# Kernel optimization log

Hardware: AMD Instinct MI355X
Metric: run time of the kernel (lower is better)

## Reference

```python
import jax, jax.numpy as jnp
import numpy as np

N = 50000
E = 800000
F_IN = 128
HID = 128
H_HID = 4
H_OUT = 6
N_CLS = 40
NEG_SLOPE = 0.2
BN_EPS = 1e-5


def gat_conv(x, src, dst, W, a_src, a_dst, bias, concat):
    # x: [N, F_in]; W: [F_in, H*C]; a_src/a_dst: [H, C]
    H, C = a_src.shape
    h = (x @ W).reshape(N, H, C)                      # [N,H,C]
    alpha_s = jnp.sum(h * a_src[None], axis=-1)       # [N,H]
    alpha_d = jnp.sum(h * a_dst[None], axis=-1)       # [N,H]
    e = jax.nn.leaky_relu(alpha_s[src] + alpha_d[dst], NEG_SLOPE)  # [E',H]
    # segment softmax over incoming edges of each dst node
    emax = jax.ops.segment_max(e, dst, num_segments=N)
    e = jnp.exp(e - emax[dst])
    denom = jax.ops.segment_sum(e, dst, num_segments=N)
    alpha = e / (denom[dst] + 1e-16)                  # [E',H]
    out = jax.ops.segment_sum(alpha[:, :, None] * h[src], dst, num_segments=N)  # [N,H,C]
    out = out.reshape(N, H * C) if concat else out.mean(axis=1)
    return out + bias


def bn_eval(x, gamma, beta, mean, var):
    return (x - mean) * (gamma / jnp.sqrt(var + BN_EPS)) + beta


def setup_inputs() -> dict:
    key = jax.random.key(0)
    ks = jax.random.split(key, 24)
    d_h = HID * H_HID  # 512
    inp = {
        'x': jax.random.normal(ks[0], (N, F_IN), jnp.float32),
        'edge_index': jax.random.randint(ks[1], (2, E), 0, N, jnp.int64),
        # layer 0: GATConv(128 -> 128, heads=4, concat)
        'W0': jax.random.normal(ks[2], (F_IN, d_h), jnp.float32) * 0.1,
        'as0': jax.random.normal(ks[3], (H_HID, HID), jnp.float32) * 0.1,
        'ad0': jax.random.normal(ks[4], (H_HID, HID), jnp.float32) * 0.1,
        'b0': jnp.zeros((d_h,), jnp.float32),
        'g0': jax.random.uniform(ks[5], (d_h,), jnp.float32, 0.5, 1.5),
        'bt0': jax.random.normal(ks[6], (d_h,), jnp.float32) * 0.1,
        'm0': jax.random.normal(ks[7], (d_h,), jnp.float32) * 0.1,
        'v0': jax.random.uniform(ks[8], (d_h,), jnp.float32, 0.5, 1.5),
        # layer 1: GATConv(512 -> 128, heads=4, concat)
        'W1': jax.random.normal(ks[9], (d_h, d_h), jnp.float32) * 0.05,
        'as1': jax.random.normal(ks[10], (H_HID, HID), jnp.float32) * 0.1,
        'ad1': jax.random.normal(ks[11], (H_HID, HID), jnp.float32) * 0.1,
        'b1': jnp.zeros((d_h,), jnp.float32),
        'g1': jax.random.uniform(ks[12], (d_h,), jnp.float32, 0.5, 1.5),
        'bt1': jax.random.normal(ks[13], (d_h,), jnp.float32) * 0.1,
        'm1': jax.random.normal(ks[14], (d_h,), jnp.float32) * 0.1,
        'v1': jax.random.uniform(ks[15], (d_h,), jnp.float32, 0.5, 1.5),
        # layer 2: GATConv(512 -> 40, heads=6, concat=False)
        'W2': jax.random.normal(ks[16], (d_h, H_OUT * N_CLS), jnp.float32) * 0.05,
        'as2': jax.random.normal(ks[17], (H_OUT, N_CLS), jnp.float32) * 0.1,
        'ad2': jax.random.normal(ks[18], (H_OUT, N_CLS), jnp.float32) * 0.1,
        'b2': jnp.zeros((N_CLS,), jnp.float32),
    }
    return inp


def reference(x, edge_index, W0, as0, ad0, b0, g0, bt0, m0, v0,
              W1, as1, ad1, b1, g1, bt1, m1, v1,
              W2, as2, ad2, b2):
    # add self loops (PyG GATConv default add_self_loops=True)
    loop = jnp.arange(N, dtype=edge_index.dtype)
    src = jnp.concatenate([edge_index[0], loop])
    dst = jnp.concatenate([edge_index[1], loop])
    # dropout is a no-op in eval mode
    h = gat_conv(x, src, dst, W0, as0, ad0, b0, concat=True)
    h = jax.nn.elu(bn_eval(h, g0, bt0, m0, v0))
    h = gat_conv(h, src, dst, W1, as1, ad1, b1, concat=True)
    h = jax.nn.elu(bn_eval(h, g1, bt1, m1, v1))
    h = gat_conv(h, src, dst, W2, as2, ad2, b2, concat=False)
    return jax.nn.log_softmax(h, axis=-1)
```

## Files before the change

### kernel.cpp

```cpp
#include <hip/hip_runtime.h>
#include <cstdint>
#include <cstddef>

#define NN 50000
#define EE 800000
#define EPQ (EE + NN)
#define NEG_SLOPE 0.2f
#define BN_EPS 1e-5f
#define SCB 256
#define NBLK ((NN + SCB - 1) / SCB)

typedef _Float16 f16x8 __attribute__((ext_vector_type(8)));
typedef _Float16 f16x4 __attribute__((ext_vector_type(4)));
typedef _Float16 f16x2 __attribute__((ext_vector_type(2)));
typedef float f32x4 __attribute__((ext_vector_type(4)));
typedef float f32x2 __attribute__((ext_vector_type(2)));
typedef unsigned int u32;
typedef unsigned char u8;
typedef unsigned short u16;

static __device__ __forceinline__ float lrelu(float x) { return x > 0.f ? x : x * NEG_SLOPE; }

static __device__ __forceinline__ u8 f32_to_fp8(float v) {
    return (u8)(__builtin_amdgcn_cvt_pk_fp8_f32(v, v, 0, false) & 0xff);
}
static __device__ __forceinline__ void fp8x4_to_f32(u32 v, float* o) {
    f32x2 lo = __builtin_amdgcn_cvt_pk_f32_fp8(v, false);
    f32x2 hi = __builtin_amdgcn_cvt_pk_f32_fp8(v, true);
    o[0] = lo[0]; o[1] = lo[1]; o[2] = hi[0]; o[3] = hi[1];
}

static __device__ __forceinline__ void gld_lds16(const void* g, void* l) {
    __builtin_amdgcn_global_load_lds((const __attribute__((address_space(1))) u32*)g,
                                     (__attribute__((address_space(3))) u32*)l, 16, 0, 0);
}

__global__ void init_count(int* __restrict__ count) {
    int i = blockIdx.x * blockDim.x + threadIdx.x;
    if (i < NN) count[i] = 1;
}

__global__ void hist_kernel(const int* __restrict__ dst, int* __restrict__ count) {
    int e = blockIdx.x * blockDim.x + threadIdx.x;
    if (e < EE) atomicAdd(&count[dst[e]], 1);
}

__global__ __launch_bounds__(SCB) void scan1(const int* __restrict__ count,
                                             int* __restrict__ excl, int* __restrict__ bsum) {
    __shared__ int tmp[SCB];
    int b = blockIdx.x, t = threadIdx.x;
    int i = b * SCB + t;
    int v = (i < NN) ? count[i] : 0;
    tmp[t] = v;
    __syncthreads();
    for (int off = 1; off < SCB; off <<= 1) {
        int u = (t >= off) ? tmp[t - off] : 0;
        __syncthreads();
        tmp[t] += u;
        __syncthreads();
    }
    if (i < NN) excl[i] = tmp[t] - v;
    if (t == SCB - 1) bsum[b] = tmp[t];
}

__global__ __launch_bounds__(256) void scan2(const int* __restrict__ bsum, int* __restrict__ boff) {
    __shared__ int tmp[256];
    int t = threadIdx.x;
    int v = (t < NBLK) ? bsum[t] : 0;
    tmp[t] = v;
    __syncthreads();
    for (int off = 1; off < 256; off <<= 1) {
        int u = (t >= off) ? tmp[t - off] : 0;
        __syncthreads();
        tmp[t] += u;
        __syncthreads();
    }
    boff[t] = tmp[t] - v;
}

__global__ void scan3(const int* __restrict__ excl, const int* __restrict__ boff,
                      int* __restrict__ rowptr, int* __restrict__ cursor) {
    int i = blockIdx.x * blockDim.x + threadIdx.x;
    if (i < NN) {
        int r = excl[i] + boff[i / SCB];
        rowptr[i] = r;
        cursor[i] = r;
    }
    if (i == NN) rowptr[NN] = EPQ;
}

__global__ void scatter_kernel(const int* __restrict__ src, const int* __restrict__ dst,
                               int* __restrict__ cursor, int* __restrict__ csrs) {
    int e = blockIdx.x * blockDim.x + threadIdx.x;
    if (e < EE) {
        int d = dst[e];
        int slot = atomicAdd(&cursor[d], 1);
        csrs[slot] = src[e];
    } else if (e < EPQ) {
        int i = e - EE;
        int slot = atomicAdd(&cursor[i], 1);
        csrs[slot] = i;
    }
}

__global__ void cast_x_kernel(const float* __restrict__ in, _Float16* __restrict__ out,
                              u32* __restrict__ outq, int n4) {
    int i = blockIdx.x * blockDim.x + threadIdx.x;
    if (i >= n4) return;
    f32x4 v = *(const f32x4*)(in + (size_t)i * 4);
    f16x4 o;
    o[0] = (_Float16)v[0]; o[1] = (_Float16)v[1]; o[2] = (_Float16)v[2]; o[3] = (_Float16)v[3];
    *(f16x4*)(out + (size_t)i * 4) = o;
    u32 q = __builtin_amdgcn_cvt_pk_fp8_f32(v[0], v[1], 0, false);
    q = __builtin_amdgcn_cvt_pk_fp8_f32(v[2], v[3], q, true);
    outq[i] = q;
}

__global__ __launch_bounds__(256) void tcast_kernel(const float* __restrict__ W,
                                                    _Float16* __restrict__ Wt, int K, int Nc) {
    __shared__ float tile[32][33];
    int bx = blockIdx.x * 32;
    int by = blockIdx.y * 32;
    int tx = threadIdx.x & 31, ty = threadIdx.x >> 5;
#pragma unroll
    for (int r = 0; r < 32; r += 8) {
        int k = by + ty + r, n = bx + tx;
        tile[ty + r][tx] = (k < K && n < Nc) ? W[(size_t)k * Nc + n] : 0.f;
    }
    __syncthreads();
#pragma unroll
    for (int r = 0; r < 32; r += 8) {
        int n = bx + ty + r, k = by + tx;
        if (n < Nc && k < K) Wt[(size_t)n * K + k] = (_Float16)tile[tx][ty + r];
    }
}

__global__ void prep_bn(const float* g0, const float* bt0, const float* m0, const float* v0,
                        const float* b0, const float* g1, const float* bt1, const float* m1,
                        const float* v1, const float* b1, float* sc01, float* sh01) {
    int t = threadIdx.x;
    const float *g, *bt, *m, *v, *b;
    int c;
    if (t < 512) { g = g0; bt = bt0; m = m0; v = v0; b = b0; c = t; }
    else         { g = g1; bt = bt1; m = m1; v = v1; b = b1; c = t - 512; }
    float s = g[c] * rsqrtf(v[c] + BN_EPS);
    sc01[t] = s;
    sh01[t] = (b[c] - m[c]) * s + bt[c];
}

__global__ __launch_bounds__(512) void prep_va(const _Float16* __restrict__ W0t,
                                               const _Float16* __restrict__ W1t,
                                               const _Float16* __restrict__ W2t,
                                               const float* __restrict__ as0,
                                               const float* __restrict__ ad0,
                                               const float* __restrict__ as1,
                                               const float* __restrict__ ad1,
                                               const float* __restrict__ as2,
                                               const float* __restrict__ ad2,
                                               float* __restrict__ va0, float* __restrict__ va1,
                                               float* __restrict__ va2) {
    int bid = blockIdx.x, t = threadIdx.x;
    if (bid < 8) {
        if (t >= 128) return;
        int j = bid, h = j & 3;
        const float* a = (j < 4 ? as0 : ad0) + h * 128;
        float s = 0.f;
        for (int c = 0; c < 128; c++) s += (float)W0t[(size_t)(h * 128 + c) * 128 + t] * a[c];
        va0[j * 128 + t] = s;
    } else if (bid < 16) {
        int j = bid - 8, h = j & 3;
        const float* a = (j < 4 ? as1 : ad1) + h * 128;
        float s = 0.f;
        for (int c = 0; c < 128; c++) s += (float)W1t[(size_t)(h * 128 + c) * 512 + t] * a[c];
        va1[j * 512 + t] = s;
    } else {
        int j = bid - 16, h = j % 6;
        const float* a = (j < 6 ? as2 : ad2) + h * 40;
        float s = 0.f;
        for (int c = 0; c < 40; c++) s += (float)W2t[(size_t)(h * 40 + c) * 512 + t] * a[c];
        va2[j * 512 + t] = s;
    }
}

template <bool BD, bool EPI, int OT>
__global__ __launch_bounds__(256) void gemm_t(const _Float16* __restrict__ A, int lda,
                                              const _Float16* __restrict__ Bt,
                                              void* __restrict__ Cv, int ldc, int M, int Nc,
                                              int K, const float* __restrict__ sc,
                                              const float* __restrict__ sh) {
    __shared__ __align__(16) _Float16 As[2][128 * 64];
    __shared__ __align__(16) _Float16 Bs[2][128 * 64];
    const int t = threadIdx.x;
    const int bm = blockIdx.x * 128;
    const int bn = blockIdx.y * 128;
    const int wid = t >> 6, lane = t & 63;
    const int wm = (wid >> 1) * 64, wn = (wid & 1) * 64;
    const int aoff = BD ? bn : 0;
    f32x4 acc[4][4] = {};
    const int nsteps = K >> 6;

    auto STAGE = [&](int buf, int k0) {
#pragma unroll
        for (int it = 0; it < 4; ++it) {
            int rbase = it * 32 + wid * 8;
            int row = rbase + (lane >> 3);
            int c8g = (lane & 7) ^ (row & 7);
            gld_lds16(A + (size_t)(bm + row) * lda + aoff + k0 + c8g * 8,
                      (char*)As[buf] + rbase * 128);
            gld_lds16(Bt + (size_t)(bn + row) * K + k0 + c8g * 8, (char*)Bs[buf] + rbase * 128);
        }
    };

    STAGE(0, 0);
    __syncthreads();
    int cur = 0;
    for (int s = 0; s < nsteps; ++s) {
        if (s + 1 < nsteps) STAGE(cur ^ 1, (s + 1) * 64);
#pragma unroll
        for (int ks = 0; ks < 2; ++ks) {
            f16x8 af[4], bf[4];
#pragma unroll
            for (int mi = 0; mi < 4; ++mi) {
                int row = wm + mi * 16 + (lane & 15);
                int c8 = (ks * 4 + (lane >> 4)) ^ (row & 7);
                af[mi] = *(const f16x8*)((const char*)As[cur] + row * 128 + c8 * 16);
            }
#pragma unroll
            for (int ni = 0; ni < 4; ++ni) {
                int row = wn + ni * 16 + (lane & 15);
                int c8 = (ks * 4 + (lane >> 4)) ^ (row & 7);
                bf[ni] = *(const f16x8*)((const char*)Bs[cur] + row * 128 + c8 * 16);
            }
#pragma unroll
            for (int mi = 0; mi < 4; ++mi)
#pragma unroll
                for (int ni = 0; ni < 4; ++ni)
                    acc[mi][ni] = __builtin_amdgcn_mfma_f32_16x16x32_f16(af[mi], bf[ni],
                                                                         acc[mi][ni], 0, 0, 0);
        }
        __syncthreads();
        cur ^= 1;
    }
    float scv[4], shv[4];
    if (EPI) {
#pragma unroll
        for (int ni = 0; ni < 4; ++ni) {
            int gcol = bn + wn + ni * 16 + (lane & 15);
            scv[ni] = sc[gcol];
            shv[ni] = sh[gcol];
        }
    }
#pragma unroll
    for (int mi = 0; mi < 4; ++mi) {
#pragma unroll
        for (int r = 0; r < 4; ++r) {
            int grow = bm + wm + mi * 16 + (lane >> 4) * 4 + r;
            if (grow < M) {
#pragma unroll
                for (int ni = 0; ni < 4; ++ni) {
                    int gcol = bn + wn + ni * 16 + (lane & 15);
                    if (gcol < Nc) {
                        float v = acc[mi][ni][r];
                        if (EPI) {
                            v = v * scv[ni] + shv[ni];
                            v = v > 0.f ? v : expm1f(v);
                        }
                        if constexpr (OT == 0) {
                            ((_Float16*)Cv)[(size_t)grow * ldc + gcol] = (_Float16)v;
                        } else {
                            ((u8*)Cv)[(size_t)grow * ldc + gcol] = f32_to_fp8(v);
                        }
                    }
                }
            }
        }
    }
}

__global__ __launch_bounds__(256) void alpha0(const _Float16* __restrict__ xh,
                                              const float* __restrict__ va0,
                                              float* __restrict__ asn, float* __restrict__ adn) {
    int wid = threadIdx.x >> 6, lane = threadIdx.x & 63;
    int i = blockIdx.x * 4 + wid;
    if (i >= NN) return;
    f16x2 x2 = *(const f16x2*)(xh + (size_t)i * 128 + lane * 2);
    float x0 = (float)x2[0], x1 = (float)x2[1];
    float p[8];
#pragma unroll
    for (int j = 0; j < 8; j++) {
        f32x2 v = *(const f32x2*)(va0 + j * 128 + lane * 2);
        p[j] = x0 * v[0] + x1 * v[1];
    }
#pragma unroll
    for (int off = 32; off; off >>= 1)
#pragma unroll
        for (int j = 0; j < 8; j++) p[j] += __shfl_xor(p[j], off);
    if (lane == 0) {
        f32x4 o0 = {p[0], p[1], p[2], p[3]}, o1 = {p[4], p[5], p[6], p[7]};
        *(f32x4*)(asn + (size_t)i * 4) = o0;
        *(f32x4*)(adn + (size_t)i * 4) = o1;
    }
}

template <int JH, int STR>
__global__ __launch_bounds__(256) void alpha12(const _Float16* __restrict__ feat,
                                               const float* __restrict__ va,
                                               float* __restrict__ asn, float* __restrict__ adn) {
    int wid = threadIdx.x >> 6, lane = threadIdx.x & 63;
    int i = blockIdx.x * 4 + wid;
    if (i >= NN) return;
    f16x8 x8 = *(const f16x8*)(feat + (size_t)i * 512 + lane * 8);
    float xf[8];
#pragma unroll
    for (int u = 0; u < 8; u++) xf[u] = (float)x8[u];
    float p[2 * JH];
#pragma unroll
    for (int j = 0; j < 2 * JH; j++) {
        const float* vr = va + j * 512 + lane * 8;
        f32x4 v0 = *(const f32x4*)vr;
        f32x4 v1 = *(const f32x4*)(vr + 4);
        p[j] = xf[0] * v0[0] + xf[1] * v0[1] + xf[2] * v0[2] + xf[3] * v0[3] +
               xf[4] * v1[0] + xf[5] * v1[1] + xf[6] * v1[2] + xf[7] * v1[3];
    }
#pragma unroll
    for (int off = 32; off; off >>= 1)
#pragma unroll
        for (int j = 0; j < 2 * JH; j++) p[j] += __shfl_xor(p[j], off);
    if (lane == 0) {
#pragma unroll
        for (int h = 0; h < JH; h++) {
            asn[(size_t)i * STR + h] = p[h];
            adn[(size_t)i * STR + h] = p[JH + h];
        }
    }
}

__global__ __launch_bounds__(256) void aggx(const u8* __restrict__ xq,
                                            const float* __restrict__ asn,
                                            const float* __restrict__ adn,
                                            const int* __restrict__ rowptr,
                                            const int* __restrict__ csr,
                                            _Float16* __restrict__ xa) {
    __shared__ __align__(8) _Float16 wsl[4][64][4];
    int wid = threadIdx.x >> 6, lane = threadIdx.x & 63;
    int i = blockIdx.x * 4 + wid;
    if (i >= NN) return;
    int start = rowptr[i], end = rowptr[i + 1], deg = end - start;
    bool fastp = deg <= 64;
    f32x4 ad = *(const f32x4*)(adn + (size_t)i * 4);
    f32x4 m4, rd4;
    if (fastp) {
        bool v = lane < deg;
        int e = start + (v ? lane : 0);
        int s = csr[e];
        f32x4 a = *(const f32x4*)(asn + (size_t)s * 4);
        f32x4 sc4, mm, wv, dn;
#pragma unroll
        for (int j = 0; j < 4; j++) { sc4[j] = v ? lrelu(a[j] + ad[j]) : -1e30f; mm[j] = sc4[j]; }
#pragma unroll
        for (int off = 32; off; off >>= 1)
#pragma unroll
            for (int j = 0; j < 4; j++) mm[j] = fmaxf(mm[j], __shfl_xor(mm[j], off));
#pragma unroll
        for (int j = 0; j < 4; j++) { wv[j] = v ? __expf(sc4[j] - mm[j]) : 0.f; dn[j] = wv[j]; }
#pragma unroll
        for (int off = 32; off; off >>= 1)
#pragma unroll
            for (int j = 0; j < 4; j++) dn[j] += __shfl_xor(dn[j], off);
        f16x4 o;
#pragma unroll
        for (int j = 0; j < 4; j++) o[j] = (_Float16)(wv[j] / (dn[j] + 1e-16f));
        *(f16x4*)&wsl[wid][lane][0] = o;
    } else {
        f32x4 mm = {-1e30f, -1e30f, -1e30f, -1e30f};
        for (int e = start + lane; e < end; e += 64) {
            int s = csr[e];
            f32x4 a = *(const f32x4*)(asn + (size_t)s * 4);
#pragma unroll
            for (int j = 0; j < 4; j++) mm[j] = fmaxf(mm[j], lrelu(a[j] + ad[j]));
        }
#pragma unroll
        for (int off = 32; off; off >>= 1)
#pragma unroll
            for (int j = 0; j < 4; j++) mm[j] = fmaxf(mm[j], __shfl_xor(mm[j], off));
        f32x4 dn = {0.f, 0.f, 0.f, 0.f};
        for (int e = start + lane; e < end; e += 64) {
            int s = csr[e];
            f32x4 a = *(const f32x4*)(asn + (size_t)s * 4);
#pragma unroll
            for (int j = 0; j < 4; j++) dn[j] += __expf(lrelu(a[j] + ad[j]) - mm[j]);
        }
#pragma unroll
        for (int off = 32; off; off >>= 1)
#pragma unroll
            for (int j = 0; j < 4; j++) dn[j] += __shfl_xor(dn[j], off);
        m4 = mm;
#pragma unroll
        for (int j = 0; j < 4; j++) rd4[j] = 1.f / (dn[j] + 1e-16f);
    }
    const char* xb = (const char*)xq + lane * 2;
    float acc[8] = {};
    for (int e = start; e < end; e++) {
        int s = csr[e];
        float w[4];
        if (fastp) {
            f16x4 wv4 = *(const f16x4*)&wsl[wid][e - start][0];
#pragma unroll
            for (int h = 0; h < 4; h++) w[h] = (float)wv4[h];
        } else {
#pragma unroll
            for (int h = 0; h < 4; h++)
                w[h] = __expf(lrelu(asn[(size_t)s * 4 + h] + ad[h]) - m4[h]) * rd4[h];
        }
        u16 pv = *(const u16*)(xb + (u32)s * 128u);
        f32x2 q = __builtin_amdgcn_cvt_pk_f32_fp8((u32)pv, false);
#pragma unroll
        for (int h = 0; h < 4; h++) {
            acc[h * 2] += w[h] * q[0];
            acc[h * 2 + 1] += w[h] * q[1];
        }
    }
#pragma unroll
    for (int h = 0; h < 4; h++) {
        f16x2 o;
        o[0] = (_Float16)acc[h * 2];
        o[1] = (_Float16)acc[h * 2 + 1];
        *(f16x2*)(xa + (size_t)i * 512 + h * 128 + lane * 2) = o;
    }
}

__global__ __launch_bounds__(256) void agg01(const u8* __restrict__ h,
                                             const float* __restrict__ asn,
                                             const float* __restrict__ adn,
                                             const int* __restrict__ rowptr,
                                             const int* __restrict__ csr,
                                             const float* __restrict__ sc,
                                             const float* __restrict__ sh,
                                             _Float16* __restrict__ out) {
    __shared__ __align__(8) _Float16 wsl[4][64][4];
    int wid = threadIdx.x >> 6, lane = threadIdx.x & 63;
    int i = blockIdx.x * 4 + wid;
    if (i >= NN) return;
    int start = rowptr[i], end = rowptr[i + 1], deg = end - start;
    bool fastp = deg <= 64;
    f32x4 ad = *(const f32x4*)(adn + (size_t)i * 4);
    f32x4 m4, rd4;
    if (fastp) {
        bool v = lane < deg;
        int e = start + (v ? lane : 0);
        int s = csr[e];
        f32x4 a = *(const f32x4*)(asn + (size_t)s * 4);
        f32x4 sc4, mm, wv, dn;
#pragma unroll
        for (int j = 0; j < 4; j++) { sc4[j] = v ? lrelu(a[j] + ad[j]) : -1e30f; mm[j] = sc4[j]; }
#pragma unroll
        for (int off = 32; off; off >>= 1)
#pragma unroll
            for (int j = 0; j < 4; j++) mm[j] = fmaxf(mm[j], __shfl_xor(mm[j], off));
#pragma unroll
        for (int j = 0; j < 4; j++) { wv[j] = v ? __expf(sc4[j] - mm[j]) : 0.f; dn[j] = wv[j]; }
#pragma unroll
        for (int off = 32; off; off >>= 1)
#pragma unroll
            for (int j = 0; j < 4; j++) dn[j] += __shfl_xor(dn[j], off);
        f16x4 o;
#pragma unroll
        for (int j = 0; j < 4; j++) o[j] = (_Float16)(wv[j] / (dn[j] + 1e-16f));
        *(f16x4*)&wsl[wid][lane][0] = o;
    } else {
        f32x4 mm = {-1e30f, -1e30f, -1e30f, -1e30f};
        for (int e = start + lane; e < end; e += 64) {
            int s = csr[e];
            f32x4 a = *(const f32x4*)(asn + (size_t)s * 4);
#pragma unroll
            for (int j = 0; j < 4; j++) mm[j] = fmaxf(mm[j], lrelu(a[j] + ad[j]));
        }
#pragma unroll
        for (int off = 32; off; off >>= 1)
#pragma unroll
            for (int j = 0; j < 4; j++) mm[j] = fmaxf(mm[j], __shfl_xor(mm[j], off));
        f32x4 dn = {0.f, 0.f, 0.f, 0.f};
        for (int e = start + lane; e < end; e += 64) {
            int s = csr[e];
            f32x4 a = *(const f32x4*)(asn + (size_t)s * 4);
#pragma unroll
            for (int j = 0; j < 4; j++) dn[j] += __expf(lrelu(a[j] + ad[j]) - mm[j]);
        }
#pragma unroll
        for (int off = 32; off; off >>= 1)
#pragma unroll
            for (int j = 0; j < 4; j++) dn[j] += __shfl_xor(dn[j], off);
        m4 = mm;
#pragma unroll
        for (int j = 0; j < 4; j++) rd4[j] = 1.f / (dn[j] + 1e-16f);
    }
    int head = lane >> 4;
    const char* hb = (const char*)h + lane * 8;
    float acc0[8] = {}, acc1[8] = {};
    int e = start;
    for (; e + 2 <= end; e += 2) {
        int s0 = csr[e], s1 = csr[e + 1];
        float w0, w1;
        if (fastp) {
            w0 = (float)wsl[wid][e - start][head];
            w1 = (float)wsl[wid][e + 1 - start][head];
        } else {
            w0 = __expf(lrelu(asn[(size_t)s0 * 4 + head] + ad[head]) - m4[head]) * rd4[head];
            w1 = __expf(lrelu(asn[(size_t)s1 * 4 + head] + ad[head]) - m4[head]) * rd4[head];
        }
        uint2 p0 = *(const uint2*)(hb + (u32)s0 * 512u);
        uint2 p1 = *(const uint2*)(hb + (u32)s1 * 512u);
        float q0[8], q1[8];
        fp8x4_to_f32(p0.x, q0); fp8x4_to_f32(p0.y, q0 + 4);
        fp8x4_to_f32(p1.x, q1); fp8x4_to_f32(p1.y, q1 + 4);
#pragma unroll
        for (int j = 0; j < 8; j++) {
            acc0[j] += w0 * q0[j];
            acc1[j] += w1 * q1[j];
        }
    }
    if (e < end) {
        int s0 = csr[e];
        float w0;
        if (fastp) w0 = (float)wsl[wid][e - start][head];
        else w0 = __expf(lrelu(asn[(size_t)s0 * 4 + head] + ad[head]) - m4[head]) * rd4[head];
        uint2 p0 = *(const uint2*)(hb + (u32)s0 * 512u);
        float q0[8];
        fp8x4_to_f32(p0.x, q0); fp8x4_to_f32(p0.y, q0 + 4);
#pragma unroll
        for (int j = 0; j < 8; j++) acc0[j] += w0 * q0[j];
    }
    int ch = lane * 8;
    f32x4 sc0 = *(const f32x4*)(sc + ch), sc1 = *(const f32x4*)(sc + ch + 4);
    f32x4 sh0 = *(const f32x4*)(sh + ch), sh1 = *(const f32x4*)(sh + ch + 4);
    f16x8 o;
#pragma unroll
    for (int j = 0; j < 8; j++) {
        float s = (j < 4) ? sc0[j] : sc1[j - 4];
        float b = (j < 4) ? sh0[j] : sh1[j - 4];
        float val = (acc0[j] + acc1[j]) * s + b;
        val = val > 0.f ? val : expm1f(val);
        o[j] = (_Float16)val;
    }
    *(f16x8*)(out + (size_t)i * 512 + ch) = o;
}

__global__ __launch_bounds__(256) void agg2f(const u8* __restrict__ h2,
                                             const float* __restrict__ asn,
                                             const float* __restrict__ adn,
                                             const int* __restrict__ rowptr,
                                             const int* __restrict__ csr,
                                             const float* __restrict__ b2,
                                             float* __restrict__ out) {
    __shared__ __align__(16) _Float16 wsl[4][64][8];
    __shared__ float sval[4][240];
    int wid = threadIdx.x >> 6, lane = threadIdx.x & 63;
    int i = blockIdx.x * 4 + wid;
    if (i < NN) {
        int start = rowptr[i], end = rowptr[i + 1], deg = end - start;
        bool fastp = deg <= 64;
        f32x4 ad0 = *(const f32x4*)(adn + (size_t)i * 8);
        f32x4 ad1 = *(const f32x4*)(adn + (size_t)i * 8 + 4);
        float adh[6] = {ad0[0], ad0[1], ad0[2], ad0[3], ad1[0], ad1[1]};
        float m6[6], rd6[6];
        if (fastp) {
            bool v = lane < deg;
            int e = start + (v ? lane : 0);
            int s = csr[e];
            f32x4 x0 = *(const f32x4*)(asn + (size_t)s * 8);
            f32x4 x1 = *(const f32x4*)(asn + (size_t)s * 8 + 4);
            float av[6] = {x0[0], x0[1], x0[2], x0[3], x1[0], x1[1]};
            float sc6[6], mm[6], wv[6], dn[6];
#pragma unroll
            for (int j = 0; j < 6; j++) {
                sc6[j] = v ? lrelu(av[j] + adh[j]) : -1e30f;
                mm[j] = sc6[j];
            }
#pragma unroll
            for (int off = 32; off; off >>= 1)
#pragma unroll
                for (int j = 0; j < 6; j++) mm[j] = fmaxf(mm[j], __shfl_xor(mm[j], off));
#pragma unroll
            for (int j = 0; j < 6; j++) { wv[j] = v ? __expf(sc6[j] - mm[j]) : 0.f; dn[j] = wv[j]; }
#pragma unroll
            for (int off = 32; off; off >>= 1)
#pragma unroll
                for (int j = 0; j < 6; j++) dn[j] += __shfl_xor(dn[j], off);
            f16x8 o;
#pragma unroll
            for (int j = 0; j < 6; j++) o[j] = (_Float16)(wv[j] / (dn[j] + 1e-16f));
            o[6] = (_Float16)0.f;
            o[7] = (_Float16)0.f;
            *(f16x8*)&wsl[wid][lane][0] = o;
        } else {
            float mm[6], dn[6];
#pragma unroll
            for (int j = 0; j < 6; j++) { mm[j] = -1e30f; dn[j] = 0.f; }
            for (int e = start + lane; e < end; e += 64) {
                int s = csr[e];
                f32x4 x0 = *(const f32x4*)(asn + (size_t)s * 8);
                f32x4 x1 = *(const f32x4*)(asn + (size_t)s * 8 + 4);
                float av[6] = {x0[0], x0[1], x0[2], x0[3], x1[0], x1[1]};
#pragma unroll
                for (int j = 0; j < 6; j++) mm[j] = fmaxf(mm[j], lrelu(av[j] + adh[j]));
            }
#pragma unroll
            for (int off = 32; off; off >>= 1)
#pragma unroll
                for (int j = 0; j < 6; j++) mm[j] = fmaxf(mm[j], __shfl_xor(mm[j], off));
            for (int e = start + lane; e < end; e += 64) {
                int s = csr[e];
                f32x4 x0 = *(const f32x4*)(asn + (size_t)s * 8);
                f32x4 x1 = *(const f32x4*)(asn + (size_t)s * 8 + 4);
                float av[6] = {x0[0], x0[1], x0[2], x0[3], x1[0], x1[1]};
#pragma unroll
                for (int j = 0; j < 6; j++) dn[j] += __expf(lrelu(av[j] + adh[j]) - mm[j]);
            }
#pragma unroll
            for (int off = 32; off; off >>= 1)
#pragma unroll
                for (int j = 0; j < 6; j++) dn[j] += __shfl_xor(dn[j], off);
#pragma unroll
            for (int j = 0; j < 6; j++) { m6[j] = mm[j]; rd6[j] = 1.f / (dn[j] + 1e-16f); }
        }
        int head = (lane < 60) ? (lane / 10) : 0;
        const char* hb = (const char*)h2 + lane * 4;
        float a0[4] = {}, a1[4] = {};
        int e = start;
        for (; e + 2 <= end; e += 2) {
            int s0 = csr[e], s1 = csr[e + 1];
            float w0, w1;
            if (fastp) {
                w0 = (float)wsl[wid][e - start][head];
                w1 = (float)wsl[wid][e + 1 - start][head];
            } else {
                w0 = __expf(lrelu(asn[(size_t)s0 * 8 + head] + adh[head]) - m6[head]) * rd6[head];
                w1 = __expf(lrelu(asn[(size_t)s1 * 8 + head] + adh[head]) - m6[head]) * rd6[head];
            }
            u32 p0 = *(const u32*)(hb + (u32)s0 * 256u);
            u32 p1 = *(const u32*)(hb + (u32)s1 * 256u);
            float q0[4], q1[4];
            fp8x4_to_f32(p0, q0);
            fp8x4_to_f32(p1, q1);
#pragma unroll
            for (int j = 0; j < 4; j++) {
                a0[j] += w0 * q0[j];
                a1[j] += w1 * q1[j];
            }
        }
        if (e < end) {
            int s0 = csr[e];
            float w0;
            if (fastp) w0 = (float)wsl[wid][e - start][head];
            else w0 = __expf(lrelu(asn[(size_t)s0 * 8 + head] + adh[head]) - m6[head]) * rd6[head];
            u32 p0 = *(const u32*)(hb + (u32)s0 * 256u);
            float q0[4];
            fp8x4_to_f32(p0, q0);
#pragma unroll
            for (int j = 0; j < 4; j++) a0[j] += w0 * q0[j];
        }
        if (lane < 60) {
#pragma unroll
            for (int j = 0; j < 4; j++) sval[wid][lane * 4 + j] = a0[j] + a1[j];
        }
    }
    __syncthreads();
    if (i < NN) {
        float v = -INFINITY;
        if (lane < 40) {
            float s = 0.f;
#pragma unroll
            for (int hh = 0; hh < 6; hh++) s += sval[wid][hh * 40 + lane];
            v = s * (1.0f / 6.0f) + b2[lane];
        }
        float mm = v;
#pragma unroll
        for (int off = 32; off; off >>= 1) mm = fmaxf(mm, __shfl_xor(mm, off));
        float se = (lane < 40) ? __expf(v - mm) : 0.f;
#pragma unroll
        for (int off = 32; off; off >>= 1) se += __shfl_xor(se, off);
        if (lane < 40) out[(size_t)i * 40 + lane] = v - mm - logf(se);
    }
}

extern "C" void kernel_launch(void* const* d_in, const int* in_sizes, int n_in,
                              void* d_out, int out_size, void* d_ws, size_t ws_size,
                              hipStream_t stream) {
    const float* x   = (const float*)d_in[0];
    const int*   ei  = (const int*)d_in[1];
    const float* W0  = (const float*)d_in[2];
    const float* as0 = (const float*)d_in[3];
    const float* ad0 = (const float*)d_in[4];
    const float* b0  = (const float*)d_in[5];
    const float* g0  = (const float*)d_in[6];
    const float* bt0 = (const float*)d_in[7];
    const float* m0  = (const float*)d_in[8];
    const float* v0  = (const float*)d_in[9];
    const float* W1  = (const float*)d_in[10];
    const float* as1 = (const float*)d_in[11];
    const float* ad1 = (const float*)d_in[12];
    const float* b1  = (const float*)d_in[13];
    const float* g1  = (const float*)d_in[14];
    const float* bt1 = (const float*)d_in[15];
    const float* m1  = (const float*)d_in[16];
    const float* v1  = (const float*)d_in[17];
    const float* W2  = (const float*)d_in[18];
    const float* as2w = (const float*)d_in[19];
    const float* ad2w = (const float*)d_in[20];
    const float* b2  = (const float*)d_in[21];
    float* out = (float*)d_out;
    const int* srcv = ei;
    const int* dstv = ei + EE;

    char* w = (char*)d_ws;
    auto carve = [&](size_t bytes) {
        char* p = w;
        w += (bytes + 255) & ~(size_t)255;
        return p;
    };
    _Float16* xh   = (_Float16*)carve((size_t)NN * 128 * 2);
    u32* xq        = (u32*)carve((size_t)NN * 128);
    _Float16* hA   = (_Float16*)carve((size_t)NN * 512 * 2);
    _Float16* actB = (_Float16*)carve((size_t)NN * 512 * 2);
    _Float16* W0t  = (_Float16*)carve((size_t)512 * 128 * 2);
    _Float16* W1t  = (_Float16*)carve((size_t)512 * 512 * 2);
    _Float16* W2t  = (_Float16*)carve((size_t)240 * 512 * 2);
    float* va0  = (float*)carve((size_t)8 * 128 * 4);
    float* va1  = (float*)carve((size_t)8 * 512 * 4);
    float* va2  = (float*)carve((size_t)12 * 512 * 4);
    float* sc01 = (float*)carve((size_t)1024 * 4);
    float* sh01 = (float*)carve((size_t)1024 * 4);
    float* asn  = (float*)carve((size_t)NN * 8 * 4);
    float* adn  = (float*)carve((size_t)NN * 8 * 4);
    int* count  = (int*)carve((size_t)(NN + 8) * 4);
    int* excl   = (int*)carve((size_t)(NN + 8) * 4);
    int* bsum   = (int*)carve((size_t)512 * 4);
    int* boff   = (int*)carve((size_t)512 * 4);
    int* rowptr = (int*)carve((size_t)(NN + 8) * 4);
    int* cursor = (int*)carve((size_t)(NN + 8) * 4);
    int* csrs   = (int*)carve((size_t)EPQ * 4);
    _Float16* xa = hA;
    u8* h1q  = (u8*)hA;
    u8* h2q  = (u8*)hA;

    init_count<<<(NN + 255) / 256, 256, 0, stream>>>(count);
    hist_kernel<<<(EE + 255) / 256, 256, 0, stream>>>(dstv, count);
    scan1<<<NBLK, SCB, 0, stream>>>(count, excl, bsum);
    scan2<<<1, 256, 0, stream>>>(bsum, boff);
    scan3<<<(NN + 256) / 256, 256, 0, stream>>>(excl, boff, rowptr, cursor);
    scatter_kernel<<<(EPQ + 255) / 256, 256, 0, stream>>>(srcv, dstv, cursor, csrs);

    cast_x_kernel<<<(NN * 128 / 4 + 255) / 256, 256, 0, stream>>>(x, xh, xq, NN * 128 / 4);
    tcast_kernel<<<dim3(16, 4), 256, 0, stream>>>(W0, W0t, 128, 512);
    tcast_kernel<<<dim3(16, 16), 256, 0, stream>>>(W1, W1t, 512, 512);
    tcast_kernel<<<dim3(8, 16), 256, 0, stream>>>(W2, W2t, 512, 240);
    prep_bn<<<1, 1024, 0, stream>>>(g0, bt0, m0, v0, b0, g1, bt1, m1, v1, b1, sc01, sh01);
    prep_va<<<28, 512, 0, stream>>>(W0t, W1t, W2t, as0, ad0, as1, ad1, as2w, ad2w, va0, va1, va2);

    const int MT = (NN + 127) / 128;
    const int NG = (NN + 3) / 4;

    alpha0<<<NG, 256, 0, stream>>>(xh, va0, asn, adn);
    aggx<<<NG, 256, 0, stream>>>((const u8*)xq, asn, adn, rowptr, csrs, xa);
    gemm_t<true, true, 0><<<dim3(MT, 4), 256, 0, stream>>>(xa, 512, W0t, actB, 512, NN, 512, 128,
                                                           sc01, sh01);

    gemm_t<false, false, 1><<<dim3(MT, 4), 256, 0, stream>>>(actB, 512, W1t, h1q, 512, NN, 512,
                                                             512, nullptr, nullptr);
    alpha12<4, 4><<<NG, 256, 0, stream>>>(actB, va1, asn, adn);
    agg01<<<NG, 256, 0, stream>>>(h1q, asn, adn, rowptr, csrs, sc01 + 512, sh01 + 512, actB);

    gemm_t<false, false, 1><<<dim3(MT, 2), 256, 0, stream>>>(actB, 512, W2t, h2q, 256, NN, 240,
                                                             512, nullptr, nullptr);
    alpha12<6, 8><<<NG, 256, 0, stream>>>(actB, va2, asn, adn);
    agg2f<<<NG, 256, 0, stream>>>(h2q, asn, adn, rowptr, csrs, b2, out);
}
```

Baseline: 603.1 us.

## Fuse prep kernels, merge x cast into alpha0, unroll aggregation loops by four

Merges the three weight transpose-cast launches into one kernel and the BN/attention-vector prep into one kernel, which cuts launch count. Folds the x cast into the alpha0 kernel so the fp16 copy of x is no longer written and read back, and alpha0 now uses fp32 x directly. Unrolls the edge loops in the three aggregation kernels to four edges per iteration so more gathers are in flight at once, at some cost in register pressure.

```diff
diff --git a/kernel.cpp b/kernel.cpp
--- a/kernel.cpp
+++ b/kernel.cpp
@@ -103,24 +103,19 @@
     }
 }
 
-__global__ void cast_x_kernel(const float* __restrict__ in, _Float16* __restrict__ out,
-                              u32* __restrict__ outq, int n4) {
-    int i = blockIdx.x * blockDim.x + threadIdx.x;
-    if (i >= n4) return;
-    f32x4 v = *(const f32x4*)(in + (size_t)i * 4);
-    f16x4 o;
-    o[0] = (_Float16)v[0]; o[1] = (_Float16)v[1]; o[2] = (_Float16)v[2]; o[3] = (_Float16)v[3];
-    *(f16x4*)(out + (size_t)i * 4) = o;
-    u32 q = __builtin_amdgcn_cvt_pk_fp8_f32(v[0], v[1], 0, false);
-    q = __builtin_amdgcn_cvt_pk_fp8_f32(v[2], v[3], q, true);
-    outq[i] = q;
-}
-
-__global__ __launch_bounds__(256) void tcast_kernel(const float* __restrict__ W,
-                                                    _Float16* __restrict__ Wt, int K, int Nc) {
+__global__ __launch_bounds__(256) void tcast_all(const float* __restrict__ W0,
+                                                 const float* __restrict__ W1,
+                                                 const float* __restrict__ W2,
+                                                 _Float16* __restrict__ W0t,
+                                                 _Float16* __restrict__ W1t,
+                                                 _Float16* __restrict__ W2t) {
     __shared__ float tile[32][33];
-    int bx = blockIdx.x * 32;
-    int by = blockIdx.y * 32;
+    int b = blockIdx.x;
+    const float* W; _Float16* Wt; int K, Nc, bx, by;
+    if (b < 64)       { W = W0; Wt = W0t; K = 128; Nc = 512; int q = b;       bx = q % 16, by = q / 16; }
+    else if (b < 320) { W = W1; Wt = W1t; K = 512; Nc = 512; int q = b - 64;  bx = q % 16, by = q / 16; }
+    else              { W = W2; Wt = W2t; K = 512; Nc = 240; int q = b - 320; bx = q % 8,  by = q / 8; }
+    bx *= 32; by *= 32;
     int tx = threadIdx.x & 31, ty = threadIdx.x >> 5;
 #pragma unroll
     for (int r = 0; r < 32; r += 8) {
@@ -135,50 +130,81 @@
     }
 }
 
-__global__ void prep_bn(const float* g0, const float* bt0, const float* m0, const float* v0,
-                        const float* b0, const float* g1, const float* bt1, const float* m1,
-                        const float* v1, const float* b1, float* sc01, float* sh01) {
-    int t = threadIdx.x;
-    const float *g, *bt, *m, *v, *b;
-    int c;
-    if (t < 512) { g = g0; bt = bt0; m = m0; v = v0; b = b0; c = t; }
-    else         { g = g1; bt = bt1; m = m1; v = v1; b = b1; c = t - 512; }
-    float s = g[c] * rsqrtf(v[c] + BN_EPS);
-    sc01[t] = s;
-    sh01[t] = (b[c] - m[c]) * s + bt[c];
-}
-
-__global__ __launch_bounds__(512) void prep_va(const _Float16* __restrict__ W0t,
-                                               const _Float16* __restrict__ W1t,
-                                               const _Float16* __restrict__ W2t,
-                                               const float* __restrict__ as0,
-                                               const float* __restrict__ ad0,
-                                               const float* __restrict__ as1,
-                                               const float* __restrict__ ad1,
-                                               const float* __restrict__ as2,
-                                               const float* __restrict__ ad2,
-                                               float* __restrict__ va0, float* __restrict__ va1,
-                                               float* __restrict__ va2) {
+__global__ __launch_bounds__(1024) void prep_all(const float* g0, const float* bt0,
+                                                 const float* m0, const float* v0, const float* b0,
+                                                 const float* g1, const float* bt1,
+                                                 const float* m1, const float* v1, const float* b1,
+                                                 const _Float16* __restrict__ W0t,
+                                                 const _Float16* __restrict__ W1t,
+                                                 const _Float16* __restrict__ W2t,
+                                                 const float* __restrict__ as0,
+                                                 const float* __restrict__ ad0,
+                                                 const float* __restrict__ as1,
+                                                 const float* __restrict__ ad1,
+                                                 const float* __restrict__ as2,
+                                                 const float* __restrict__ ad2,
+                                                 float* sc01, float* sh01, float* va0, float* va1,
+                                                 float* va2) {
     int bid = blockIdx.x, t = threadIdx.x;
-    if (bid < 8) {
+    if (bid == 0) {
+        const float *g, *bt, *m, *v, *b;
+        int c;
+        if (t < 512) { g = g0; bt = bt0; m = m0; v = v0; b = b0; c = t; }
+        else         { g = g1; bt = bt1; m = m1; v = v1; b = b1; c = t - 512; }
+        float s = g[c] * rsqrtf(v[c] + BN_EPS);
+        sc01[t] = s;
+        sh01[t] = (b[c] - m[c]) * s + bt[c];
+        return;
+    }
+    int vb = bid - 1;
+    if (vb < 8) {
         if (t >= 128) return;
-        int j = bid, h = j & 3;
+        int j = vb, h = j & 3;
         const float* a = (j < 4 ? as0 : ad0) + h * 128;
         float s = 0.f;
         for (int c = 0; c < 128; c++) s += (float)W0t[(size_t)(h * 128 + c) * 128 + t] * a[c];
         va0[j * 128 + t] = s;
-    } else if (bid < 16) {
-        int j = bid - 8, h = j & 3;
+    } else if (vb < 16) {
+        if (t >= 512) return;
+        int j = vb - 8, h = j & 3;
         const float* a = (j < 4 ? as1 : ad1) + h * 128;
         float s = 0.f;
         for (int c = 0; c < 128; c++) s += (float)W1t[(size_t)(h * 128 + c) * 512 + t] * a[c];
         va1[j * 512 + t] = s;
     } else {
-        int j = bid - 16, h = j % 6;
+        if (t >= 512) return;
+        int j = vb - 16, h = j % 6;
         const float* a = (j < 6 ? as2 : ad2) + h * 40;
         float s = 0.f;
         for (int c = 0; c < 40; c++) s += (float)W2t[(size_t)(h * 40 + c) * 512 + t] * a[c];
         va2[j * 512 + t] = s;
+    }
+}
+
+__global__ __launch_bounds__(256) void castx_alpha0(const float* __restrict__ x,
+                                                    const float* __restrict__ va0,
+                                                    u8* __restrict__ xq, float* __restrict__ asn,
+                                                    float* __restrict__ adn) {
+    int wid = threadIdx.x >> 6, lane = threadIdx.x & 63;
+    int i = blockIdx.x * 4 + wid;
+    if (i >= NN) return;
+    f32x2 xv = *(const f32x2*)(x + (size_t)i * 128 + lane * 2);
+    u32 q = __builtin_amdgcn_cvt_pk_fp8_f32(xv[0], xv[1], 0, false);
+    *((u16*)(xq + (size_t)i * 128) + lane) = (u16)(q & 0xffff);
+    float p[8];
+#pragma unroll
+    for (int j = 0; j < 8; j++) {
+        f32x2 v = *(const f32x2*)(va0 + j * 128 + lane * 2);
+        p[j] = xv[0] * v[0] + xv[1] * v[1];
+    }
+#pragma unroll
+    for (int off = 32; off; off >>= 1)
+#pragma unroll
+        for (int j = 0; j < 8; j++) p[j] += __shfl_xor(p[j], off);
+    if (lane == 0) {
+        f32x4 o0 = {p[0], p[1], p[2], p[3]}, o1 = {p[4], p[5], p[6], p[7]};
+        *(f32x4*)(asn + (size_t)i * 4) = o0;
+        *(f32x4*)(adn + (size_t)i * 4) = o1;
     }
 }
 
@@ -274,31 +300,6 @@
                 }
             }
         }
-    }
-}
-
-__global__ __launch_bounds__(256) void alpha0(const _Float16* __restrict__ xh,
-                                              const float* __restrict__ va0,
-                                              float* __restrict__ asn, float* __restrict__ adn) {
-    int wid = threadIdx.x >> 6, lane = threadIdx.x & 63;
-    int i = blockIdx.x * 4 + wid;
-    if (i >= NN) return;
-    f16x2 x2 = *(const f16x2*)(xh + (size_t)i * 128 + lane * 2);
-    float x0 = (float)x2[0], x1 = (float)x2[1];
-    float p[8];
-#pragma unroll
-    for (int j = 0; j < 8; j++) {
-        f32x2 v = *(const f32x2*)(va0 + j * 128 + lane * 2);
-        p[j] = x0 * v[0] + x1 * v[1];
-    }
-#pragma unroll
-    for (int off = 32; off; off >>= 1)
-#pragma unroll
-        for (int j = 0; j < 8; j++) p[j] += __shfl_xor(p[j], off);
-    if (lane == 0) {
-        f32x4 o0 = {p[0], p[1], p[2], p[3]}, o1 = {p[4], p[5], p[6], p[7]};
-        *(f32x4*)(asn + (size_t)i * 4) = o0;
-        *(f32x4*)(adn + (size_t)i * 4) = o1;
     }
 }
 
@@ -400,18 +401,40 @@
     }
     const char* xb = (const char*)xq + lane * 2;
     float acc[8] = {};
-    for (int e = start; e < end; e++) {
+    int e = start;
+    auto getw = [&](int ee, int ss, float* w) {
+        if (fastp) {
+            f16x4 wv4 = *(const f16x4*)&wsl[wid][ee - start][0];
+#pragma unroll
+            for (int h = 0; h < 4; h++) w[h] = (float)wv4[h];
+        } else {
+#pragma unroll
+            for (int h = 0; h < 4; h++)
+                w[h] = __expf(lrelu(asn[(size_t)ss * 4 + h] + ad[h]) - m4[h]) * rd4[h];
+        }
+    };
+    for (; e + 4 <= end; e += 4) {
+        int s0 = csr[e], s1 = csr[e + 1], s2 = csr[e + 2], s3 = csr[e + 3];
+        u16 pv0 = *(const u16*)(xb + (u32)s0 * 128u);
+        u16 pv1 = *(const u16*)(xb + (u32)s1 * 128u);
+        u16 pv2 = *(const u16*)(xb + (u32)s2 * 128u);
+        u16 pv3 = *(const u16*)(xb + (u32)s3 * 128u);
+        float w0[4], w1[4], w2[4], w3[4];
+        getw(e, s0, w0); getw(e + 1, s1, w1); getw(e + 2, s2, w2); getw(e + 3, s3, w3);
+        f32x2 q0 = __builtin_amdgcn_cvt_pk_f32_fp8((u32)pv0, false);
+        f32x2 q1 = __builtin_amdgcn_cvt_pk_f32_fp8((u32)pv1, false);
+        f32x2 q2 = __builtin_amdgcn_cvt_pk_f32_fp8((u32)pv2, false);
+        f32x2 q3 = __builtin_amdgcn_cvt_pk_f32_fp8((u32)pv3, false);
+#pragma unroll
+        for (int h = 0; h < 4; h++) {
+            acc[h * 2]     += w0[h] * q0[0] + w1[h] * q1[0] + w2[h] * q2[0] + w3[h] * q3[0];
+            acc[h * 2 + 1] += w0[h] * q0[1] + w1[h] * q1[1] + w2[h] * q2[1] + w3[h] * q3[1];
+        }
+    }
+    for (; e < end; e++) {
         int s = csr[e];
         float w[4];
-        if (fastp) {
-            f16x4 wv4 = *(const f16x4*)&wsl[wid][e - start][0];
-#pragma unroll
-            for (int h = 0; h < 4; h++) w[h] = (float)wv4[h];
-        } else {
-#pragma unroll
-            for (int h = 0; h < 4; h++)
-                w[h] = __expf(lrelu(asn[(size_t)s * 4 + h] + ad[h]) - m4[h]) * rd4[h];
-        }
+        getw(e, s, w);
         u16 pv = *(const u16*)(xb + (u32)s * 128u);
         f32x2 q = __builtin_amdgcn_cvt_pk_f32_fp8((u32)pv, false);
 #pragma unroll
@@ -498,32 +521,32 @@
     const char* hb = (const char*)h + lane * 8;
     float acc0[8] = {}, acc1[8] = {};
     int e = start;
-    for (; e + 2 <= end; e += 2) {
-        int s0 = csr[e], s1 = csr[e + 1];
-        float w0, w1;
-        if (fastp) {
-            w0 = (float)wsl[wid][e - start][head];
-            w1 = (float)wsl[wid][e + 1 - start][head];
-        } else {
-            w0 = __expf(lrelu(asn[(size_t)s0 * 4 + head] + ad[head]) - m4[head]) * rd4[head];
-            w1 = __expf(lrelu(asn[(size_t)s1 * 4 + head] + ad[head]) - m4[head]) * rd4[head];
-        }
+    auto getw1 = [&](int ee, int ss) -> float {
+        if (fastp) return (float)wsl[wid][ee - start][head];
+        return __expf(lrelu(asn[(size_t)ss * 4 + head] + ad[head]) - m4[head]) * rd4[head];
+    };
+    for (; e + 4 <= end; e += 4) {
+        int s0 = csr[e], s1 = csr[e + 1], s2 = csr[e + 2], s3 = csr[e + 3];
         uint2 p0 = *(const uint2*)(hb + (u32)s0 * 512u);
         uint2 p1 = *(const uint2*)(hb + (u32)s1 * 512u);
-        float q0[8], q1[8];
+        uint2 p2 = *(const uint2*)(hb + (u32)s2 * 512u);
+        uint2 p3 = *(const uint2*)(hb + (u32)s3 * 512u);
+        float w0 = getw1(e, s0), w1 = getw1(e + 1, s1);
+        float w2 = getw1(e + 2, s2), w3 = getw1(e + 3, s3);
+        float q0[8], q1[8], q2[8], q3[8];
         fp8x4_to_f32(p0.x, q0); fp8x4_to_f32(p0.y, q0 + 4);
         fp8x4_to_f32(p1.x, q1); fp8x4_to_f32(p1.y, q1 + 4);
+        fp8x4_to_f32(p2.x, q2); fp8x4_to_f32(p2.y, q2 + 4);
+        fp8x4_to_f32(p3.x, q3); fp8x4_to_f32(p3.y, q3 + 4);
 #pragma unroll
         for (int j = 0; j < 8; j++) {
-            acc0[j] += w0 * q0[j];
-            acc1[j] += w1 * q1[j];
-        }
-    }
-    if (e < end) {
+            acc0[j] += w0 * q0[j] + w2 * q2[j];
+            acc1[j] += w1 * q1[j] + w3 * q3[j];
+        }
+    }
+    for (; e < end; e++) {
         int s0 = csr[e];
-        float w0;
-        if (fastp) w0 = (float)wsl[wid][e - start][head];
-        else w0 = __expf(lrelu(asn[(size_t)s0 * 4 + head] + ad[head]) - m4[head]) * rd4[head];
+        float w0 = getw1(e, s0);
         uint2 p0 = *(const uint2*)(hb + (u32)s0 * 512u);
         float q0[8];
         fp8x4_to_f32(p0.x, q0); fp8x4_to_f32(p0.y, q0 + 4);
@@ -627,32 +650,32 @@
         const char* hb = (const char*)h2 + lane * 4;
         float a0[4] = {}, a1[4] = {};
         int e = start;
-        for (; e + 2 <= end; e += 2) {
-            int s0 = csr[e], s1 = csr[e + 1];
-            float w0, w1;
-            if (fastp) {
-                w0 = (float)wsl[wid][e - start][head];
-                w1 = (float)wsl[wid][e + 1 - start][head];
-            } else {
-                w0 = __expf(lrelu(asn[(size_t)s0 * 8 + head] + adh[head]) - m6[head]) * rd6[head];
-                w1 = __expf(lrelu(asn[(size_t)s1 * 8 + head] + adh[head]) - m6[head]) * rd6[head];
-            }
+        auto getw1 = [&](int ee, int ss) -> float {
+            if (fastp) return (float)wsl[wid][ee - start][head];
+            return __expf(lrelu(asn[(size_t)ss * 8 + head] + adh[head]) - m6[head]) * rd6[head];
+        };
+        for (; e + 4 <= end; e += 4) {
+            int s0 = csr[e], s1 = csr[e + 1], s2 = csr[e + 2], s3 = csr[e + 3];
             u32 p0 = *(const u32*)(hb + (u32)s0 * 256u);
             u32 p1 = *(const u32*)(hb + (u32)s1 * 256u);
-            float q0[4], q1[4];
+            u32 p2 = *(const u32*)(hb + (u32)s2 * 256u);
+            u32 p3 = *(const u32*)(hb + (u32)s3 * 256u);
+            float w0 = getw1(e, s0), w1 = getw1(e + 1, s1);
+            float w2 = getw1(e + 2, s2), w3 = getw1(e + 3, s3);
+            float q0[4], q1[4], q2[4], q3[4];
             fp8x4_to_f32(p0, q0);
             fp8x4_to_f32(p1, q1);
+            fp8x4_to_f32(p2, q2);
+            fp8x4_to_f32(p3, q3);
 #pragma unroll
             for (int j = 0; j < 4; j++) {
-                a0[j] += w0 * q0[j];
-                a1[j] += w1 * q1[j];
+                a0[j] += w0 * q0[j] + w2 * q2[j];
+                a1[j] += w1 * q1[j] + w3 * q3[j];
             }
         }
-        if (e < end) {
+        for (; e < end; e++) {
             int s0 = csr[e];
-            float w0;
-            if (fastp) w0 = (float)wsl[wid][e - start][head];
-            else w0 = __expf(lrelu(asn[(size_t)s0 * 8 + head] + adh[head]) - m6[head]) * rd6[head];
+            float w0 = getw1(e, s0);
             u32 p0 = *(const u32*)(hb + (u32)s0 * 256u);
             float q0[4];
             fp8x4_to_f32(p0, q0);
@@ -718,7 +741,6 @@
         w += (bytes + 255) & ~(size_t)255;
         return p;
     };
-    _Float16* xh   = (_Float16*)carve((size_t)NN * 128 * 2);
     u32* xq        = (u32*)carve((size_t)NN * 128);
     _Float16* hA   = (_Float16*)carve((size_t)NN * 512 * 2);
     _Float16* actB = (_Float16*)carve((size_t)NN * 512 * 2);
@@ -750,17 +772,14 @@
     scan3<<<(NN + 256) / 256, 256, 0, stream>>>(excl, boff, rowptr, cursor);
     scatter_kernel<<<(EPQ + 255) / 256, 256, 0, stream>>>(srcv, dstv, cursor, csrs);
 
-    cast_x_kernel<<<(NN * 128 / 4 + 255) / 256, 256, 0, stream>>>(x, xh, xq, NN * 128 / 4);
-    tcast_kernel<<<dim3(16, 4), 256, 0, stream>>>(W0, W0t, 128, 512);
-    tcast_kernel<<<dim3(16, 16), 256, 0, stream>>>(W1, W1t, 512, 512);
-    tcast_kernel<<<dim3(8, 16), 256, 0, stream>>>(W2, W2t, 512, 240);
-    prep_bn<<<1, 1024, 0, stream>>>(g0, bt0, m0, v0, b0, g1, bt1, m1, v1, b1, sc01, sh01);
-    prep_va<<<28, 512, 0, stream>>>(W0t, W1t, W2t, as0, ad0, as1, ad1, as2w, ad2w, va0, va1, va2);
+    tcast_all<<<448, 256, 0, stream>>>(W0, W1, W2, W0t, W1t, W2t);
+    prep_all<<<29, 1024, 0, stream>>>(g0, bt0, m0, v0, b0, g1, bt1, m1, v1, b1, W0t, W1t, W2t,
+                                      as0, ad0, as1, ad1, as2w, ad2w, sc01, sh01, va0, va1, va2);
 
     const int MT = (NN + 127) / 128;
     const int NG = (NN + 3) / 4;
 
-    alpha0<<<NG, 256, 0, stream>>>(xh, va0, asn, adn);
+    castx_alpha0<<<NG, 256, 0, stream>>>(x, va0, (u8*)xq, asn, adn);
     aggx<<<NG, 256, 0, stream>>>((const u8*)xq, asn, adn, rowptr, csrs, xa);
     gemm_t<true, true, 0><<<dim3(MT, 4), 256, 0, stream>>>(xa, 512, W0t, actB, 512, NN, 512, 128,
                                                            sc01, sh01);
```

After: 569.2 us. 5.6% less time.
